# Kernel optimization log

Hardware: AMD Instinct MI355X
Metric: run time of the kernel (lower is better)

Reference implementation:

```python
import jax, jax.numpy as jnp
import numpy as np
import math

B, S, D = 4, 4096, 1024
H, DH = 16, 64          # n_heads x head_dim = d_model
INTER = 4096            # intermediate_size
CAP = int(S * 0.25)     # MoD capacity = capacity_factor * seq_len = 1024


def rmsnorm(x, w, eps=1e-6):
    return x * jax.lax.rsqrt(jnp.mean(x * x, axis=-1, keepdims=True) + eps) * w


def setup_inputs() -> dict:
    key = jax.random.key(0)
    ks = jax.random.split(key, 12)
    s = 1.0 / math.sqrt(D)
    return {
        "hidden_states": jax.random.normal(ks[0], (B, S, D), jnp.float32),
        "ssm_norm_w": jnp.ones((D,), jnp.float32),
        "ssm_a": jax.random.normal(ks[1], (D,), jnp.float32),
        "ssm_gain": jax.random.normal(ks[2], (D,), jnp.float32) * 0.1,
        "router_w": jax.random.normal(ks[3], (D,), jnp.float32) * s,
        "attn_norm_w": jnp.ones((D,), jnp.float32),
        "wq": jax.random.normal(ks[4], (D, D), jnp.float32) * s,
        "wk": jax.random.normal(ks[5], (D, D), jnp.float32) * s,
        "wv": jax.random.normal(ks[6], (D, D), jnp.float32) * s,
        "wo": jax.random.normal(ks[7], (D, D), jnp.float32) * s,
        "ffn_norm_w": jnp.ones((D,), jnp.float32),
        "w1": jax.random.normal(ks[8], (D, INTER), jnp.float32) * s,
        "w2": jax.random.normal(ks[9], (INTER, D), jnp.float32) / math.sqrt(INTER),
    }


def reference(hidden_states, ssm_norm_w, ssm_a, ssm_gain, router_w, attn_norm_w,
              wq, wk, wv, wo, ffn_norm_w, w1, w2):
    # --- SSM layer (pre-norm diagonal linear recurrence + residual) ---
    xb = rmsnorm(hidden_states, ssm_norm_w)
    decay = jax.nn.sigmoid(ssm_a)  # [D] per-channel state decay

    def step(hprev, xt):  # xt: [B, D]
        hnew = decay * hprev + (1.0 - decay) * xt
        return hnew, hnew

    _, ys = jax.lax.scan(step, jnp.zeros((B, D), jnp.float32), jnp.swapaxes(xb, 0, 1))
    h = hidden_states + jnp.swapaxes(ys, 0, 1) * ssm_gain  # [B, S, D]

    # --- MoD router: pick top-CAP tokens per sequence ---
    scores = jnp.einsum('bsd,d->bs', h, router_w)            # [B, S]
    _, idx = jax.lax.top_k(scores, CAP)                      # [B, C]
    idx = jnp.sort(idx, axis=-1)                             # keep causal order
    weights = jax.nn.sigmoid(jnp.take_along_axis(scores, idx, axis=1))  # [B, C]
    aux_loss = jnp.mean(jax.nn.sigmoid(scores))              # router load aux

    # --- gather selected tokens -> attention ---
    sel = jnp.take_along_axis(h, idx[:, :, None], axis=1)    # [B, C, D]
    xn = rmsnorm(sel, attn_norm_w)
    q = (xn @ wq).reshape(B, CAP, H, DH)
    k = (xn @ wk).reshape(B, CAP, H, DH)
    v = (xn @ wv).reshape(B, CAP, H, DH)
    att = jnp.einsum('bqhd,bkhd->bhqk', q, k) / math.sqrt(DH)
    causal = jnp.tril(jnp.ones((CAP, CAP), bool))
    att = jnp.where(causal, att, jnp.float32(-1e30))
    p = jax.nn.softmax(att, axis=-1)
    o = jnp.einsum('bhqk,bkhd->bqhd', p, v).reshape(B, CAP, D)
    attn_out = o @ wo                                        # [B, C, D]

    # --- weighted scatter_add back onto the residual stream ---
    b_idx = jnp.arange(B)[:, None]
    h = h.at[b_idx, idx].add(attn_out * weights[:, :, None])

    # --- dense FFN residual (non-MoE layer) ---
    xf = rmsnorm(h, ffn_norm_w)
    h = h + jax.nn.silu(xf @ w1) @ w2
    return h, aux_loss
```

## Files before the change

### kernel.cpp

```cpp
#include <hip/hip_runtime.h>

typedef unsigned short u16;
typedef unsigned int   u32;
typedef __attribute__((ext_vector_type(4))) float f32x4;
typedef __attribute__((ext_vector_type(8))) __bf16 bf16x8;
typedef __attribute__((ext_vector_type(8))) unsigned short u16x8;

#define DEV __device__ __forceinline__

DEV u16 f2bf(float f){
  u32 u = __builtin_bit_cast(u32, f);
  u32 r = (u + 0x7fffu + ((u >> 16) & 1u)) >> 16;
  return (u16)r;
}

DEV f32x4 mfma16(bf16x8 a, bf16x8 b, f32x4 c){
  return __builtin_amdgcn_mfma_f32_16x16x32_bf16(a, b, c, 0, 0, 0);
}

DEV void gload16(const void* g, void* l){
  __builtin_amdgcn_global_load_lds((const __attribute__((address_space(1))) u32*)g,
                                   (__attribute__((address_space(3))) u32*)l, 16, 0, 0);
}

DEV int swz16(int r, int g){ return r*64 + 8*(g ^ (r&7) ^ ((r>>3)&7)); }
DEV int swze (int r, int e){ return r*64 + (e&7) + 8*(((e>>3) ^ (r&7) ^ ((r>>3)&7))); }

__global__ __launch_bounds__(256) void transpose_cast(const float* __restrict__ src,
                                                      u16* __restrict__ dst, int R, int C){
  __shared__ float tile[32][33];
  int r  = threadIdx.x >> 3;
  int c4 = (threadIdx.x & 7) * 4;
  int r0 = blockIdx.x * 32, c0 = blockIdx.y * 32;
  float4 v = *(const float4*)&src[(size_t)(r0 + r) * C + c0 + c4];
  tile[r][c4+0] = v.x; tile[r][c4+1] = v.y; tile[r][c4+2] = v.z; tile[r][c4+3] = v.w;
  __syncthreads();
  ushort4 o;
  o.x = f2bf(tile[c4+0][r]);
  o.y = f2bf(tile[c4+1][r]);
  o.z = f2bf(tile[c4+2][r]);
  o.w = f2bf(tile[c4+3][r]);
  *(ushort4*)&dst[(size_t)(c0 + r) * R + r0 + c4] = o;
}

__global__ __launch_bounds__(256) void rms_inv_k(const float* __restrict__ x, float* __restrict__ inv){
  int row  = blockIdx.x * 4 + (threadIdx.x >> 6);
  int lane = threadIdx.x & 63;
  const float* p = x + (size_t)row * 1024;
  float ss = 0.f;
  #pragma unroll
  for (int j = 0; j < 4; ++j){
    float4 v = *(const float4*)&p[lane*4 + j*256];
    ss += v.x*v.x + v.y*v.y + v.z*v.z + v.w*v.w;
  }
  #pragma unroll
  for (int o = 1; o < 64; o <<= 1) ss += __shfl_xor(ss, o);
  if (lane == 0) inv[row] = 1.f / sqrtf(ss * (1.f/1024.f) + 1e-6f);
}

__global__ __launch_bounds__(1024) void ssm_a_k(const float* __restrict__ hid, const float* __restrict__ invr,
    const float* __restrict__ nw, const float* __restrict__ av, float* __restrict__ Fc){
  int c = blockIdx.x & 63, b = blockIdx.x >> 6;
  int d = threadIdx.x;
  float w   = nw[d];
  float dec = 1.f/(1.f + expf(-av[d]));
  float od  = 1.f - dec;
  const float* hp = hid + ((size_t)b*4096 + c*64)*1024 + d;
  const float* ip = invr + b*4096 + c*64;
  float hs = 0.f;
  for (int i = 0; i < 64; ++i)
    hs = dec*hs + od*(hp[(size_t)i*1024] * ip[i] * w);
  Fc[((size_t)b*64 + c)*1024 + d] = hs;
}
__global__ __launch_bounds__(1024) void ssm_b_k(const float* __restrict__ Fc, float* __restrict__ Init,
                                                const float* __restrict__ av){
  int b = blockIdx.x, d = threadIdx.x;
  float dec = 1.f/(1.f + expf(-av[d]));
  float dl  = powf(dec, 64.f);
  float cur = 0.f;
  for (int c = 0; c < 64; ++c){
    size_t o = ((size_t)b*64 + c)*1024 + d;
    Init[o] = cur;
    cur = dl*cur + Fc[o];
  }
}
__global__ __launch_bounds__(1024) void ssm_c_k(const float* __restrict__ hid, const float* __restrict__ invr,
    const float* __restrict__ nw, const float* __restrict__ av, const float* __restrict__ gn,
    const float* __restrict__ Init, float* __restrict__ hout){
  int c = blockIdx.x & 63, b = blockIdx.x >> 6;
  int d = threadIdx.x;
  float w   = nw[d];
  float g   = gn[d];
  float dec = 1.f/(1.f + expf(-av[d]));
  float od  = 1.f - dec;
  size_t rowoff = ((size_t)b*4096 + c*64)*1024 + d;
  const float* hp = hid + rowoff;
  float* op = hout + rowoff;
  const float* ip = invr + b*4096 + c*64;
  float hs = Init[((size_t)b*64 + c)*1024 + d];
  for (int i = 0; i < 64; ++i){
    float hv = hp[(size_t)i*1024];
    hs = dec*hs + od*(hv * ip[i] * w);
    op[(size_t)i*1024] = hv + hs*g;
  }
}

__global__ __launch_bounds__(256) void score_k(const float* __restrict__ h, const float* __restrict__ rw,
                                               float* __restrict__ sc){
  int row  = blockIdx.x * 4 + (threadIdx.x >> 6);
  int lane = threadIdx.x & 63;
  const float* p = h + (size_t)row * 1024;
  float s = 0.f;
  #pragma unroll
  for (int j = 0; j < 4; ++j){
    float4 v = *(const float4*)&p[lane*4 + j*256];
    float4 w = *(const float4*)&rw[lane*4 + j*256];
    s += v.x*w.x + v.y*w.y + v.z*w.z + v.w*w.w;
  }
  #pragma unroll
  for (int o = 1; o < 64; o <<= 1) s += __shfl_xor(s, o);
  if (lane == 0) sc[row] = s;
}

__global__ __launch_bounds__(256) void aux_k(const float* __restrict__ sc, float* __restrict__ out){
  __shared__ float red[256];
  int tid = threadIdx.x;
  float s = 0.f;
  for (int i = tid; i < 16384; i += 256) s += 1.f/(1.f + expf(-sc[i]));
  red[tid] = s; __syncthreads();
  for (int o = 128; o > 0; o >>= 1){ if (tid < o) red[tid] += red[tid+o]; __syncthreads(); }
  if (tid == 0) out[0] = red[0] * (1.f/16384.f);
}

__global__ __launch_bounds__(1024) void topk_k(const float* __restrict__ sc, int* __restrict__ idx,
                                               float* __restrict__ wsel){
  __shared__ float sv[4096];
  __shared__ int   si[4096];
  int b = blockIdx.x, tid = threadIdx.x;
  for (int i = tid; i < 4096; i += 1024){ sv[i] = sc[b*4096 + i]; si[i] = i; }
  __syncthreads();
  for (int k = 2; k <= 4096; k <<= 1)
    for (int j = k >> 1; j > 0; j >>= 1){
      for (int i = tid; i < 4096; i += 1024){
        int p = i ^ j;
        if (p > i){
          float vi = sv[i], vp = sv[p];
          int ii = si[i], ip = si[p];
          bool before = (vi > vp) || (vi == vp && ii < ip);
          bool desc = ((i & k) == 0);
          if (desc ? !before : before){ sv[i]=vp; sv[p]=vi; si[i]=ip; si[p]=ii; }
        }
      }
      __syncthreads();
    }
  for (int k = 2; k <= 1024; k <<= 1)
    for (int j = k >> 1; j > 0; j >>= 1){
      int i = tid, p = i ^ j;
      if (p > i){
        int a = si[i], c = si[p];
        bool asc = ((i & k) == 0);
        if (asc ? (a > c) : (a < c)){ si[i] = c; si[p] = a; }
      }
      __syncthreads();
    }
  int t = si[tid];
  idx[b*1024 + tid]  = t;
  wsel[b*1024 + tid] = 1.f/(1.f + expf(-sc[b*4096 + t]));
}

__global__ __launch_bounds__(256) void rownorm_bf16_k(const float* __restrict__ src, const float* __restrict__ w,
    u16* __restrict__ dst, const int* __restrict__ gidx, int base){
  int row  = blockIdx.x * 4 + (threadIdx.x >> 6);
  int lane = threadIdx.x & 63;
  size_t srow;
  if (gidx){ int b = row >> 10; srow = (size_t)b*4096 + gidx[row]; }
  else srow = (size_t)(base + row);
  const float* p = src + srow*1024;
  float4 v[4]; float ss = 0.f;
  #pragma unroll
  for (int j = 0; j < 4; ++j){
    v[j] = *(const float4*)&p[lane*4 + j*256];
    ss += v[j].x*v[j].x + v[j].y*v[j].y + v[j].z*v[j].z + v[j].w*v[j].w;
  }
  #pragma unroll
  for (int o = 1; o < 64; o <<= 1) ss += __shfl_xor(ss, o);
  float inv = 1.f / sqrtf(ss * (1.f/1024.f) + 1e-6f);
  #pragma unroll
  for (int j = 0; j < 4; ++j){
    float4 wv = *(const float4*)&w[lane*4 + j*256];
    ushort4 o4;
    o4.x = f2bf(v[j].x*inv*wv.x);
    o4.y = f2bf(v[j].y*inv*wv.y);
    o4.z = f2bf(v[j].z*inv*wv.z);
    o4.w = f2bf(v[j].w*inv*wv.w);
    *(ushort4*)&dst[(size_t)row*1024 + lane*4 + j*256] = o4;
  }
}

template<int BN, int WM, int WN, int EPI, int MINW>
__global__ __launch_bounds__(512, MINW) void gemm8(const u16* __restrict__ A, const u16* __restrict__ BT,
    u16* __restrict__ Cb, float* __restrict__ Cf, int M, int N, int K,
    const int* __restrict__ gidx, const float* __restrict__ wsel){
  constexpr int WROWS = 256 / WM;
  constexpr int WCOLS = BN / WN;
  constexpr int MI = WROWS / 16;
  constexpr int NI = WCOLS / 16;
  constexpr int BR = BN / 64;
  __shared__ u16 As[2][256*64];
  __shared__ u16 Bs[2][BN*64];

  int tid = threadIdx.x, wave = tid >> 6, lane = tid & 63;
  int lr = lane & 15, lg = lane >> 4;
  int wm = wave / WN, wn = wave % WN;

  int lin = blockIdx.x + gridDim.x * blockIdx.y;
  int nwg = gridDim.x * gridDim.y;
  int q = nwg >> 3, r = nwg & 7;
  int xc = lin & 7, of = lin >> 3;
  int s = (xc < r ? xc*(q+1) : r*(q+1) + (xc-r)*q) + of;
  int bm = s % gridDim.x, bn = s / gridDim.x;

  f32x4 zero4 = {0.f,0.f,0.f,0.f};
  f32x4 acc[MI][NI];
  #pragma unroll
  for (int mi = 0; mi < MI; ++mi)
    #pragma unroll
    for (int ni = 0; ni < NI; ++ni) acc[mi][ni] = zero4;

  int srow = (wave << 3) + (lane >> 3);
  int glog = (lane & 7) ^ (srow & 7);
  const size_t Kb = (size_t)K * 2;
  const char* aptr[4];
  const char* bptr[BR];
  #pragma unroll
  for (int rr = 0; rr < 4; ++rr)
    aptr[rr] = (const char*)A + (size_t)(bm*256 + rr*64 + srow) * Kb + glog*16;
  #pragma unroll
  for (int rr = 0; rr < BR; ++rr)
    bptr[rr] = (const char*)BT + (size_t)(bn*BN + rr*64 + srow) * Kb + glog*16;

  int nkt = K >> 6;
  #pragma unroll
  for (int rr = 0; rr < 4; ++rr) gload16(aptr[rr], &As[0][(rr*64 + (wave<<3))*64]);
  #pragma unroll
  for (int rr = 0; rr < BR; ++rr) gload16(bptr[rr], &Bs[0][(rr*64 + (wave<<3))*64]);
  __syncthreads();

  for (int kt = 0; kt < nkt; ++kt){
    int bi = kt & 1;
    if (kt + 1 < nkt){
      size_t koff = (size_t)(kt + 1) << 7;
      #pragma unroll
      for (int rr = 0; rr < 4; ++rr) gload16(aptr[rr] + koff, &As[bi^1][(rr*64 + (wave<<3))*64]);
      #pragma unroll
      for (int rr = 0; rr < BR; ++rr) gload16(bptr[rr] + koff, &Bs[bi^1][(rr*64 + (wave<<3))*64]);
    }
    __builtin_amdgcn_sched_barrier(0);

    bf16x8 bfrag[NI][2];
    #pragma unroll
    for (int ni = 0; ni < NI; ++ni)
      #pragma unroll
      for (int ks = 0; ks < 2; ++ks){
        int row = wn*WCOLS + ni*16 + lr;
        int gl = (ks*4 + lg) ^ (row & 7);
        bfrag[ni][ks] = *(const bf16x8*)&Bs[bi][row*64 + gl*8];
      }
    #pragma unroll
    for (int mh = 0; mh < 2; ++mh){
      bf16x8 afrag[MI/2][2];
      #pragma unroll
      for (int i = 0; i < MI/2; ++i)
        #pragma unroll
        for (int ks = 0; ks < 2; ++ks){
          int row = wm*WROWS + (mh*(MI/2) + i)*16 + lr;
          int gl = (ks*4 + lg) ^ (row & 7);
          afrag[i][ks] = *(const bf16x8*)&As[bi][row*64 + gl*8];
        }
      #pragma unroll
      for (int i = 0; i < MI/2; ++i)
        #pragma unroll
        for (int ni = 0; ni < NI; ++ni){
          f32x4 a = acc[mh*(MI/2)+i][ni];
          a = mfma16(afrag[i][0], bfrag[ni][0], a);
          a = mfma16(afrag[i][1], bfrag[ni][1], a);
          acc[mh*(MI/2)+i][ni] = a;
        }
    }
    __syncthreads();
  }

  #pragma unroll
  for (int mi = 0; mi < MI; ++mi){
    int rb = bm*256 + wm*WROWS + mi*16 + lg*4;
    #pragma unroll
    for (int ni = 0; ni < NI; ++ni){
      int col = bn*BN + wn*WCOLS + ni*16 + lr;
      f32x4 v = acc[mi][ni];
      if constexpr (EPI == 0){
        #pragma unroll
        for (int t = 0; t < 4; ++t) Cb[(size_t)(rb+t)*N + col] = f2bf(v[t]);
      } else if constexpr (EPI == 1){
        #pragma unroll
        for (int t = 0; t < 4; ++t){ float x = v[t]; Cb[(size_t)(rb+t)*N + col] = f2bf(x / (1.f + expf(-x))); }
      } else if constexpr (EPI == 2){
        #pragma unroll
        for (int t = 0; t < 4; ++t) Cf[(size_t)(rb+t)*N + col] += v[t];
      } else {
        #pragma unroll
        for (int t = 0; t < 4; ++t){
          int rr = rb + t;
          int bb = rr >> 10;
          float* hr = Cf + ((size_t)bb*4096 + gidx[rr])*1024;
          hr[col] += v[t] * wsel[rr];
        }
      }
    }
  }
}

DEV void attn_body(const u16* __restrict__ qkv, u16* __restrict__ obuf,
                   u16* Ks, u16* Vt, u16* Pl, int b, int hh, int qt){
  int tid = threadIdx.x;
  int wave = tid >> 6, lane = tid & 63;
  int lr = lane & 15, lg = lane >> 4;

  const u16* qrow = qkv + (size_t)(b*1024 + qt*64 + wave*16 + lr)*3072 + hh*64;
  bf16x8 qf0 = *(const bf16x8*)(qrow + lg*8);
  bf16x8 qf1 = *(const bf16x8*)(qrow + 32 + lg*8);

  f32x4 zero4 = {0.f,0.f,0.f,0.f};
  f32x4 oacc[4];
  #pragma unroll
  for (int d = 0; d < 4; ++d) oacc[d] = zero4;
  float m[4], s[4];
  #pragma unroll
  for (int t = 0; t < 4; ++t){ m[t] = -INFINITY; s[t] = 0.f; }

  int key0 = tid >> 3,         ce0 = (tid & 7) * 8;
  int key1 = (tid + 256) >> 3, ce1 = ((tid + 256) & 7) * 8;
  u16x8 kreg0, kreg1, vreg0, vreg1;

  const u16* kvbase = qkv + (size_t)(b*1024)*3072 + 1024 + hh*64;
  {
    const u16* g0 = kvbase + (size_t)key0*3072 + ce0;
    const u16* g1 = kvbase + (size_t)key1*3072 + ce1;
    kreg0 = *(const u16x8*)g0;  vreg0 = *(const u16x8*)(g0 + 1024);
    kreg1 = *(const u16x8*)g1;  vreg1 = *(const u16x8*)(g1 + 1024);
  }

  for (int kt = 0; kt <= qt; ++kt){
    __syncthreads();
    *(u16x8*)&Ks[swz16(key0, ce0 >> 3)] = kreg0;
    *(u16x8*)&Ks[swz16(key1, ce1 >> 3)] = kreg1;
    #pragma unroll
    for (int j = 0; j < 8; ++j) Vt[swze(ce0 + j, key0)] = vreg0[j];
    #pragma unroll
    for (int j = 0; j < 8; ++j) Vt[swze(ce1 + j, key1)] = vreg1[j];
    __syncthreads();
    if (kt < qt){
      const u16* g0 = kvbase + (size_t)((kt+1)*64 + key0)*3072 + ce0;
      const u16* g1 = kvbase + (size_t)((kt+1)*64 + key1)*3072 + ce1;
      kreg0 = *(const u16x8*)g0;  vreg0 = *(const u16x8*)(g0 + 1024);
      kreg1 = *(const u16x8*)g1;  vreg1 = *(const u16x8*)(g1 + 1024);
    }

    float sv[4][4];
    #pragma unroll
    for (int kb = 0; kb < 4; ++kb){
      f32x4 sa = zero4;
      bf16x8 k0f = *(const bf16x8*)&Ks[swz16(kb*16 + lr, lg)];
      bf16x8 k1f = *(const bf16x8*)&Ks[swz16(kb*16 + lr, 4 + lg)];
      sa = mfma16(qf0, k0f, sa);
      sa = mfma16(qf1, k1f, sa);
      #pragma unroll
      for (int t = 0; t < 4; ++t) sv[kb][t] = sa[t]*0.125f;
    }
    if (kt == qt){
      #pragma unroll
      for (int kb = 0; kb < 4; ++kb){
        int keyg = kb*16 + lr;
        #pragma unroll
        for (int t = 0; t < 4; ++t){
          int qg = wave*16 + lg*4 + t;
          if (keyg > qg) sv[kb][t] = -1e30f;
        }
      }
    }
    float mn[4], scale[4];
    #pragma unroll
    for (int t = 0; t < 4; ++t){
      float tm = fmaxf(fmaxf(sv[0][t], sv[1][t]), fmaxf(sv[2][t], sv[3][t]));
      #pragma unroll
      for (int o = 1; o < 16; o <<= 1) tm = fmaxf(tm, __shfl_xor(tm, o));
      mn[t] = fmaxf(m[t], tm);
      scale[t] = expf(m[t] - mn[t]);
      m[t] = mn[t];
    }
    float ps[4] = {0.f,0.f,0.f,0.f};
    #pragma unroll
    for (int kb = 0; kb < 4; ++kb)
      #pragma unroll
      for (int t = 0; t < 4; ++t){
        float p = expf(sv[kb][t] - mn[t]);
        ps[t] += p;
        Pl[wave*1024 + swze(lg*4 + t, kb*16 + lr)] = f2bf(p);
      }
    #pragma unroll
    for (int t = 0; t < 4; ++t){
      #pragma unroll
      for (int o = 1; o < 16; o <<= 1) ps[t] += __shfl_xor(ps[t], o);
      s[t] = s[t]*scale[t] + ps[t];
    }
    #pragma unroll
    for (int d = 0; d < 4; ++d){
      f32x4 v = oacc[d];
      #pragma unroll
      for (int t = 0; t < 4; ++t) v[t] *= scale[t];
      oacc[d] = v;
    }
    bf16x8 pa0 = *(const bf16x8*)&Pl[wave*1024 + swz16(lr, lg)];
    bf16x8 pa1 = *(const bf16x8*)&Pl[wave*1024 + swz16(lr, 4 + lg)];
    #pragma unroll
    for (int d = 0; d < 4; ++d){
      bf16x8 v0 = *(const bf16x8*)&Vt[swz16(d*16 + lr, lg)];
      bf16x8 v1 = *(const bf16x8*)&Vt[swz16(d*16 + lr, 4 + lg)];
      oacc[d] = mfma16(pa0, v0, oacc[d]);
      oacc[d] = mfma16(pa1, v1, oacc[d]);
    }
  }
  #pragma unroll
  for (int d = 0; d < 4; ++d)
    #pragma unroll
    for (int t = 0; t < 4; ++t){
      int qrel = qt*64 + wave*16 + lg*4 + t;
      float val = oacc[d][t] / s[t];
      obuf[(size_t)(b*1024 + qrel)*1024 + hh*64 + d*16 + lr] = f2bf(val);
    }
}

__global__ __launch_bounds__(256) void attn_k(const u16* __restrict__ qkv, u16* __restrict__ obuf){
  __shared__ u16 Ks[64*64];
  __shared__ u16 Vt[64*64];
  __shared__ u16 Pl[4*16*64];
  int blk = blockIdx.x;
  int qp = blk & 7;
  int hh = (blk >> 3) & 15;
  int b  = blk >> 7;
  attn_body(qkv, obuf, Ks, Vt, Pl, b, hh, qp);
  attn_body(qkv, obuf, Ks, Vt, Pl, b, hh, 15 - qp);
}

extern "C" void kernel_launch(void* const* d_in, const int* in_sizes, int n_in,
                              void* d_out, int out_size, void* d_ws, size_t ws_size,
                              hipStream_t stream) {
  const float* hid    = (const float*)d_in[0];
  const float* nssm   = (const float*)d_in[1];
  const float* ssma   = (const float*)d_in[2];
  const float* ssmg   = (const float*)d_in[3];
  const float* routw  = (const float*)d_in[4];
  const float* nattn  = (const float*)d_in[5];
  const float* wq     = (const float*)d_in[6];
  const float* wk     = (const float*)d_in[7];
  const float* wv     = (const float*)d_in[8];
  const float* wo     = (const float*)d_in[9];
  const float* nffn   = (const float*)d_in[10];
  const float* w1     = (const float*)d_in[11];
  const float* w2     = (const float*)d_in[12];

  float* hbuf = (float*)d_out;
  char* wsb = (char*)d_ws;
  u16*   wqkvT  = (u16*)(wsb + 0);
  u16*   woT    = (u16*)(wsb + 6291456);
  u16*   w1T    = (u16*)(wsb + 8388608);
  u16*   w2T    = (u16*)(wsb + 16777216);
  float* invr   = (float*)(wsb + 25165824);
  float* scores = (float*)(wsb + 25231360);
  float* Fc     = (float*)(wsb + 25296896);
  float* Init   = (float*)(wsb + 26345472);
  int*   idxb   = (int*)(wsb + 27394048);
  float* wselb  = (float*)(wsb + 27410432);
  u16*   xn     = (u16*)(wsb + 27426816);
  u16*   qkv    = (u16*)(wsb + 35815424);
  u16*   obuf   = (u16*)(wsb + 60981248);
  u16*   xf     = (u16*)(wsb + 27394048);
  u16*   act    = (u16*)(wsb + 35782656);

  transpose_cast<<<dim3(32,32),  256, 0, stream>>>(wq, wqkvT,              1024, 1024);
  transpose_cast<<<dim3(32,32),  256, 0, stream>>>(wk, wqkvT + 1048576,    1024, 1024);
  transpose_cast<<<dim3(32,32),  256, 0, stream>>>(wv, wqkvT + 2097152,    1024, 1024);
  transpose_cast<<<dim3(32,32),  256, 0, stream>>>(wo, woT,                1024, 1024);
  transpose_cast<<<dim3(32,128), 256, 0, stream>>>(w1, w1T,                1024, 4096);
  transpose_cast<<<dim3(128,32), 256, 0, stream>>>(w2, w2T,                4096, 1024);

  rms_inv_k<<<4096, 256, 0, stream>>>(hid, invr);
  ssm_a_k<<<256, 1024, 0, stream>>>(hid, invr, nssm, ssma, Fc);
  ssm_b_k<<<4,   1024, 0, stream>>>(Fc, Init, ssma);
  ssm_c_k<<<256, 1024, 0, stream>>>(hid, invr, nssm, ssma, ssmg, Init, hbuf);

  score_k<<<4096, 256, 0, stream>>>(hbuf, routw, scores);
  aux_k<<<1, 256, 0, stream>>>(scores, hbuf + 16777216);
  topk_k<<<4, 1024, 0, stream>>>(scores, idxb, wselb);

  rownorm_bf16_k<<<1024, 256, 0, stream>>>(hbuf, nattn, xn, idxb, 0);
  gemm8<256,2,4,0,2><<<dim3(16,12), 512, 0, stream>>>(xn, wqkvT, qkv, nullptr, 4096, 3072, 1024, nullptr, nullptr);
  attn_k<<<512, 256, 0, stream>>>(qkv, obuf);
  gemm8<64,4,2,3,4><<<dim3(16,16), 512, 0, stream>>>(obuf, woT, nullptr, hbuf, 4096, 1024, 1024, idxb, wselb);

  for (int ch = 0; ch < 4; ++ch){
    int m0 = ch * 4096;
    rownorm_bf16_k<<<1024, 256, 0, stream>>>(hbuf, nffn, xf, nullptr, m0);
    gemm8<256,2,4,1,2><<<dim3(16,16), 512, 0, stream>>>(xf, w1T, act, nullptr, 4096, 4096, 1024, nullptr, nullptr);
    gemm8<64,4,2,2,4><<<dim3(16,16), 512, 0, stream>>>(act, w2T, nullptr, hbuf + (size_t)m0*1024, 4096, 1024, 4096, nullptr, nullptr);
  }
  (void)in_sizes; (void)n_in; (void)out_size; (void)ws_size;
}
```

Measured before the change: 829.8 us.

## Triple-buffer GEMM pipeline, retile GEMMs, and parallel-scan SSM chunk carry

The GEMM kernel moves from double- to triple-buffered LDS staging. Explicit vmcnt waits and raw s_barrier keep two k-tiles in flight, and s_setprio raises priority around the MFMA block. Each GEMM launch gets new tile shapes (BM/BN templated, 128x128 or 256x128), and all A fragments are loaded at once. The SSM chunk-carry kernel becomes a wave-level Hillis-Steele scan over the 64 chunks across 256 blocks instead of a serial loop in 4 blocks. The costs are higher LDS and register use, which can lower occupancy, and a slightly different floating-point rounding order in the scan.

```diff
diff --git a/kernel.cpp b/kernel.cpp
--- a/kernel.cpp
+++ b/kernel.cpp
@@ -22,6 +22,8 @@
   __builtin_amdgcn_global_load_lds((const __attribute__((address_space(1))) u32*)g,
                                    (__attribute__((address_space(3))) u32*)l, 16, 0, 0);
 }
+
+template<int N> DEV void waitvm(){ asm volatile("s_waitcnt vmcnt(%0)" :: "n"(N) : "memory"); }
 
 DEV int swz16(int r, int g){ return r*64 + 8*(g ^ (r&7) ^ ((r>>3)&7)); }
 DEV int swze (int r, int e){ return r*64 + (e&7) + 8*(((e>>3) ^ (r&7) ^ ((r>>3)&7))); }
@@ -74,15 +76,23 @@
 }
 __global__ __launch_bounds__(1024) void ssm_b_k(const float* __restrict__ Fc, float* __restrict__ Init,
                                                 const float* __restrict__ av){
-  int b = blockIdx.x, d = threadIdx.x;
+  int b  = blockIdx.x >> 6;
+  int dg = blockIdx.x & 63;
+  int dl = threadIdx.x >> 6;
+  int c  = threadIdx.x & 63;
+  int d  = dg*16 + dl;
   float dec = 1.f/(1.f + expf(-av[d]));
-  float dl  = powf(dec, 64.f);
-  float cur = 0.f;
-  for (int c = 0; c < 64; ++c){
-    size_t o = ((size_t)b*64 + c)*1024 + d;
-    Init[o] = cur;
-    cur = dl*cur + Fc[o];
-  }
+  float a = powf(dec, 64.f);
+  float x = Fc[((size_t)(b*64 + c))*1024 + d];
+  float coef = a;
+  #pragma unroll
+  for (int s = 1; s < 64; s <<= 1){
+    float prev = __shfl_up(x, s, 64);
+    if (c >= s) x += coef * prev;
+    coef *= coef;
+  }
+  float ex = __shfl_up(x, 1, 64);
+  Init[((size_t)(b*64 + c))*1024 + d] = (c > 0) ? ex : 0.f;
 }
 __global__ __launch_bounds__(1024) void ssm_c_k(const float* __restrict__ hid, const float* __restrict__ invr,
     const float* __restrict__ nw, const float* __restrict__ av, const float* __restrict__ gn,
@@ -197,17 +207,19 @@
   }
 }
 
-template<int BN, int WM, int WN, int EPI, int MINW>
-__global__ __launch_bounds__(512, MINW) void gemm8(const u16* __restrict__ A, const u16* __restrict__ BT,
+template<int BM, int BN, int WM, int WN, int EPI>
+__global__ __launch_bounds__(512, 1) void gemmp(const u16* __restrict__ A, const u16* __restrict__ BT,
     u16* __restrict__ Cb, float* __restrict__ Cf, int M, int N, int K,
     const int* __restrict__ gidx, const float* __restrict__ wsel){
-  constexpr int WROWS = 256 / WM;
+  constexpr int WROWS = BM / WM;
   constexpr int WCOLS = BN / WN;
   constexpr int MI = WROWS / 16;
   constexpr int NI = WCOLS / 16;
+  constexpr int AR = BM / 64;
   constexpr int BR = BN / 64;
-  __shared__ u16 As[2][256*64];
-  __shared__ u16 Bs[2][BN*64];
+  constexpr int LPS = AR + BR;
+  __shared__ u16 As[3][BM*64];
+  __shared__ u16 Bs[3][BN*64];
 
   int tid = threadIdx.x, wave = tid >> 6, lane = tid & 63;
   int lr = lane & 15, lg = lane >> 4;
@@ -215,10 +227,10 @@
 
   int lin = blockIdx.x + gridDim.x * blockIdx.y;
   int nwg = gridDim.x * gridDim.y;
-  int q = nwg >> 3, r = nwg & 7;
+  int q8 = nwg >> 3, r8 = nwg & 7;
   int xc = lin & 7, of = lin >> 3;
-  int s = (xc < r ? xc*(q+1) : r*(q+1) + (xc-r)*q) + of;
-  int bm = s % gridDim.x, bn = s / gridDim.x;
+  int sw = (xc < r8 ? xc*(q8+1) : r8*(q8+1) + (xc-r8)*q8) + of;
+  int bm = sw % gridDim.x, bn = sw / gridDim.x;
 
   f32x4 zero4 = {0.f,0.f,0.f,0.f};
   f32x4 acc[MI][NI];
@@ -230,32 +242,34 @@
   int srow = (wave << 3) + (lane >> 3);
   int glog = (lane & 7) ^ (srow & 7);
   const size_t Kb = (size_t)K * 2;
-  const char* aptr[4];
+  const char* aptr[AR];
   const char* bptr[BR];
   #pragma unroll
-  for (int rr = 0; rr < 4; ++rr)
-    aptr[rr] = (const char*)A + (size_t)(bm*256 + rr*64 + srow) * Kb + glog*16;
+  for (int rr = 0; rr < AR; ++rr)
+    aptr[rr] = (const char*)A + (size_t)(bm*BM + rr*64 + srow) * Kb + glog*16;
   #pragma unroll
   for (int rr = 0; rr < BR; ++rr)
     bptr[rr] = (const char*)BT + (size_t)(bn*BN + rr*64 + srow) * Kb + glog*16;
 
   int nkt = K >> 6;
-  #pragma unroll
-  for (int rr = 0; rr < 4; ++rr) gload16(aptr[rr], &As[0][(rr*64 + (wave<<3))*64]);
-  #pragma unroll
-  for (int rr = 0; rr < BR; ++rr) gload16(bptr[rr], &Bs[0][(rr*64 + (wave<<3))*64]);
-  __syncthreads();
-
-  for (int kt = 0; kt < nkt; ++kt){
-    int bi = kt & 1;
-    if (kt + 1 < nkt){
-      size_t koff = (size_t)(kt + 1) << 7;
-      #pragma unroll
-      for (int rr = 0; rr < 4; ++rr) gload16(aptr[rr] + koff, &As[bi^1][(rr*64 + (wave<<3))*64]);
-      #pragma unroll
-      for (int rr = 0; rr < BR; ++rr) gload16(bptr[rr] + koff, &Bs[bi^1][(rr*64 + (wave<<3))*64]);
-    }
-    __builtin_amdgcn_sched_barrier(0);
+
+#define STAGE(T, BUF) do { \
+    size_t koff = (size_t)(T) << 7; \
+    _Pragma("unroll") \
+    for (int rr = 0; rr < AR; ++rr) gload16(aptr[rr] + koff, &As[BUF][(rr*64 + (wave<<3))*64]); \
+    _Pragma("unroll") \
+    for (int rr = 0; rr < BR; ++rr) gload16(bptr[rr] + koff, &Bs[BUF][(rr*64 + (wave<<3))*64]); \
+  } while(0)
+
+  STAGE(0, 0);
+  STAGE(1, 1);
+
+  for (int t = 0; t < nkt; ++t){
+    int q = t % 3;
+    if (t + 2 < nkt){ STAGE(t+2, (t+2)%3); waitvm<2*LPS>(); }
+    else if (t + 1 < nkt){ waitvm<LPS>(); }
+    else { waitvm<0>(); }
+    __builtin_amdgcn_s_barrier();
 
     bf16x8 bfrag[NI][2];
     #pragma unroll
@@ -264,35 +278,35 @@
       for (int ks = 0; ks < 2; ++ks){
         int row = wn*WCOLS + ni*16 + lr;
         int gl = (ks*4 + lg) ^ (row & 7);
-        bfrag[ni][ks] = *(const bf16x8*)&Bs[bi][row*64 + gl*8];
-      }
-    #pragma unroll
-    for (int mh = 0; mh < 2; ++mh){
-      bf16x8 afrag[MI/2][2];
-      #pragma unroll
-      for (int i = 0; i < MI/2; ++i)
-        #pragma unroll
-        for (int ks = 0; ks < 2; ++ks){
-          int row = wm*WROWS + (mh*(MI/2) + i)*16 + lr;
-          int gl = (ks*4 + lg) ^ (row & 7);
-          afrag[i][ks] = *(const bf16x8*)&As[bi][row*64 + gl*8];
-        }
-      #pragma unroll
-      for (int i = 0; i < MI/2; ++i)
-        #pragma unroll
-        for (int ni = 0; ni < NI; ++ni){
-          f32x4 a = acc[mh*(MI/2)+i][ni];
-          a = mfma16(afrag[i][0], bfrag[ni][0], a);
-          a = mfma16(afrag[i][1], bfrag[ni][1], a);
-          acc[mh*(MI/2)+i][ni] = a;
-        }
-    }
-    __syncthreads();
-  }
+        bfrag[ni][ks] = *(const bf16x8*)&Bs[q][row*64 + gl*8];
+      }
+    bf16x8 afrag[MI][2];
+    #pragma unroll
+    for (int mi = 0; mi < MI; ++mi)
+      #pragma unroll
+      for (int ks = 0; ks < 2; ++ks){
+        int row = wm*WROWS + mi*16 + lr;
+        int gl = (ks*4 + lg) ^ (row & 7);
+        afrag[mi][ks] = *(const bf16x8*)&As[q][row*64 + gl*8];
+      }
+    __builtin_amdgcn_s_setprio(1);
+    #pragma unroll
+    for (int mi = 0; mi < MI; ++mi)
+      #pragma unroll
+      for (int ni = 0; ni < NI; ++ni){
+        f32x4 a = acc[mi][ni];
+        a = mfma16(afrag[mi][0], bfrag[ni][0], a);
+        a = mfma16(afrag[mi][1], bfrag[ni][1], a);
+        acc[mi][ni] = a;
+      }
+    __builtin_amdgcn_s_setprio(0);
+    __builtin_amdgcn_s_barrier();
+  }
+#undef STAGE
 
   #pragma unroll
   for (int mi = 0; mi < MI; ++mi){
-    int rb = bm*256 + wm*WROWS + mi*16 + lg*4;
+    int rb = bm*BM + wm*WROWS + mi*16 + lg*4;
     #pragma unroll
     for (int ni = 0; ni < NI; ++ni){
       int col = bn*BN + wn*WCOLS + ni*16 + lr;
@@ -495,7 +509,7 @@
 
   rms_inv_k<<<4096, 256, 0, stream>>>(hid, invr);
   ssm_a_k<<<256, 1024, 0, stream>>>(hid, invr, nssm, ssma, Fc);
-  ssm_b_k<<<4,   1024, 0, stream>>>(Fc, Init, ssma);
+  ssm_b_k<<<256, 1024, 0, stream>>>(Fc, Init, ssma);
   ssm_c_k<<<256, 1024, 0, stream>>>(hid, invr, nssm, ssma, ssmg, Init, hbuf);
 
   score_k<<<4096, 256, 0, stream>>>(hbuf, routw, scores);
@@ -503,15 +517,15 @@
   topk_k<<<4, 1024, 0, stream>>>(scores, idxb, wselb);
 
   rownorm_bf16_k<<<1024, 256, 0, stream>>>(hbuf, nattn, xn, idxb, 0);
-  gemm8<256,2,4,0,2><<<dim3(16,12), 512, 0, stream>>>(xn, wqkvT, qkv, nullptr, 4096, 3072, 1024, nullptr, nullptr);
+  gemmp<128,128,2,4,0><<<dim3(32,24), 512, 0, stream>>>(xn, wqkvT, qkv, nullptr, 4096, 3072, 1024, nullptr, nullptr);
   attn_k<<<512, 256, 0, stream>>>(qkv, obuf);
-  gemm8<64,4,2,3,4><<<dim3(16,16), 512, 0, stream>>>(obuf, woT, nullptr, hbuf, 4096, 1024, 1024, idxb, wselb);
+  gemmp<128,128,2,4,3><<<dim3(32,8), 512, 0, stream>>>(obuf, woT, nullptr, hbuf, 4096, 1024, 1024, idxb, wselb);
 
   for (int ch = 0; ch < 4; ++ch){
     int m0 = ch * 4096;
     rownorm_bf16_k<<<1024, 256, 0, stream>>>(hbuf, nffn, xf, nullptr, m0);
-    gemm8<256,2,4,1,2><<<dim3(16,16), 512, 0, stream>>>(xf, w1T, act, nullptr, 4096, 4096, 1024, nullptr, nullptr);
-    gemm8<64,4,2,2,4><<<dim3(16,16), 512, 0, stream>>>(act, w2T, nullptr, hbuf + (size_t)m0*1024, 4096, 1024, 4096, nullptr, nullptr);
+    gemmp<256,128,4,2,1><<<dim3(16,32), 512, 0, stream>>>(xf, w1T, act, nullptr, 4096, 4096, 1024, nullptr, nullptr);
+    gemmp<128,128,2,4,2><<<dim3(32,8), 512, 0, stream>>>(act, w2T, nullptr, hbuf + (size_t)m0*1024, 4096, 1024, 4096, nullptr, nullptr);
   }
   (void)in_sizes; (void)n_in; (void)out_size; (void)ws_size;
 }
```

After: 874.9 us. 1.05x slower.

## Add deep-pipelined FFN up GEMM, parallel SSM chunk scan, and K-from-global attention

Applied to the files above, without the earlier changes.

Adds a new GEMM kernel for the W1 projection. It uses four K-slice LDS stages with counted vmcnt waits and raised MFMA priority, so loads stay in flight while compute runs. The SSM carry pass changes from a 4-block serial loop into a 256-block wave-shuffle parallel scan over chunks. Attention now reads K fragments directly from global memory instead of staging them in LDS, and triple-buffers V in LDS to drop one barrier per tile. The risks are more global traffic for K in attention and higher register pressure in the new GEMM.

```diff
diff --git a/kernel.cpp b/kernel.cpp
--- a/kernel.cpp
+++ b/kernel.cpp
@@ -22,6 +22,8 @@
   __builtin_amdgcn_global_load_lds((const __attribute__((address_space(1))) u32*)g,
                                    (__attribute__((address_space(3))) u32*)l, 16, 0, 0);
 }
+
+template<int N> DEV void waitvm(){ asm volatile("s_waitcnt vmcnt(%0)" :: "n"(N) : "memory"); }
 
 DEV int swz16(int r, int g){ return r*64 + 8*(g ^ (r&7) ^ ((r>>3)&7)); }
 DEV int swze (int r, int e){ return r*64 + (e&7) + 8*(((e>>3) ^ (r&7) ^ ((r>>3)&7))); }
@@ -74,15 +76,23 @@
 }
 __global__ __launch_bounds__(1024) void ssm_b_k(const float* __restrict__ Fc, float* __restrict__ Init,
                                                 const float* __restrict__ av){
-  int b = blockIdx.x, d = threadIdx.x;
+  int b  = blockIdx.x >> 6;
+  int dg = blockIdx.x & 63;
+  int dl = threadIdx.x >> 6;
+  int c  = threadIdx.x & 63;
+  int d  = dg*16 + dl;
   float dec = 1.f/(1.f + expf(-av[d]));
-  float dl  = powf(dec, 64.f);
-  float cur = 0.f;
-  for (int c = 0; c < 64; ++c){
-    size_t o = ((size_t)b*64 + c)*1024 + d;
-    Init[o] = cur;
-    cur = dl*cur + Fc[o];
-  }
+  float a = powf(dec, 64.f);
+  float x = Fc[((size_t)(b*64 + c))*1024 + d];
+  float coef = a;
+  #pragma unroll
+  for (int s = 1; s < 64; s <<= 1){
+    float prev = __shfl_up(x, s, 64);
+    if (c >= s) x += coef * prev;
+    coef *= coef;
+  }
+  float ex = __shfl_up(x, 1, 64);
+  Init[((size_t)(b*64 + c))*1024 + d] = (c > 0) ? ex : 0.f;
 }
 __global__ __launch_bounds__(1024) void ssm_c_k(const float* __restrict__ hid, const float* __restrict__ invr,
     const float* __restrict__ nw, const float* __restrict__ av, const float* __restrict__ gn,
@@ -215,10 +225,10 @@
 
   int lin = blockIdx.x + gridDim.x * blockIdx.y;
   int nwg = gridDim.x * gridDim.y;
-  int q = nwg >> 3, r = nwg & 7;
+  int q8 = nwg >> 3, r8 = nwg & 7;
   int xc = lin & 7, of = lin >> 3;
-  int s = (xc < r ? xc*(q+1) : r*(q+1) + (xc-r)*q) + of;
-  int bm = s % gridDim.x, bn = s / gridDim.x;
+  int sw = (xc < r8 ? xc*(q8+1) : r8*(q8+1) + (xc-r8)*q8) + of;
+  int bm = sw % gridDim.x, bn = sw / gridDim.x;
 
   f32x4 zero4 = {0.f,0.f,0.f,0.f};
   f32x4 acc[MI][NI];
@@ -319,8 +329,113 @@
   }
 }
 
+template<int EPI>
+__global__ __launch_bounds__(512, 2) void gemmdp(const u16* __restrict__ A, const u16* __restrict__ BT,
+    u16* __restrict__ Cb, float* __restrict__ Cf, int M, int N, int K,
+    const int* __restrict__ gidx, const float* __restrict__ wsel){
+  __shared__ u16 As[2][2][256*32];
+  __shared__ u16 Bs[2][2][256*32];
+  int tid = threadIdx.x, wave = tid >> 6, lane = tid & 63;
+  int lr = lane & 15, lg = lane >> 4;
+  int wm = wave >> 2, wn = wave & 3;
+
+  int lin = blockIdx.x + gridDim.x * blockIdx.y;
+  int nwg = gridDim.x * gridDim.y;
+  int q8 = nwg >> 3, r8 = nwg & 7;
+  int xc = lin & 7, of = lin >> 3;
+  int sw = (xc < r8 ? xc*(q8+1) : r8*(q8+1) + (xc-r8)*q8) + of;
+  int bm = sw % gridDim.x, bn = sw / gridDim.x;
+
+  f32x4 zero4 = {0.f,0.f,0.f,0.f};
+  f32x4 acc[8][4];
+  #pragma unroll
+  for (int mi = 0; mi < 8; ++mi)
+    #pragma unroll
+    for (int ni = 0; ni < 4; ++ni) acc[mi][ni] = zero4;
+
+  int sr = lane >> 2;
+  int sg = lane & 3;
+  const size_t Kb = (size_t)K * 2;
+  const char* abase[2]; const char* bbase[2];
+  #pragma unroll
+  for (int rr = 0; rr < 2; ++rr){
+    int ga = bm*256 + rr*128 + wave*16 + sr;
+    int gb = bn*256 + rr*128 + wave*16 + sr;
+    abase[rr] = (const char*)A  + (size_t)ga * Kb + (sg ^ (ga & 3))*16;
+    bbase[rr] = (const char*)BT + (size_t)gb * Kb + (sg ^ (gb & 3))*16;
+  }
+  int NP = K >> 5;
+
+#define STG(Q) do { \
+    int _b = ((Q)>>1)&1, _s = (Q)&1; \
+    size_t _ko = (size_t)(Q) << 6; \
+    gload16(abase[0] + _ko, &As[_b][_s][(wave*16)*32]); \
+    gload16(abase[1] + _ko, &As[_b][_s][(128 + wave*16)*32]); \
+    gload16(bbase[0] + _ko, &Bs[_b][_s][(wave*16)*32]); \
+    gload16(bbase[1] + _ko, &Bs[_b][_s][(128 + wave*16)*32]); \
+  } while(0)
+
+#define PHASE(P, NW) do { \
+    waitvm<NW>(); \
+    __builtin_amdgcn_s_barrier(); \
+    __builtin_amdgcn_sched_barrier(0); \
+    const u16* _Asl = &As[((P)>>1)&1][(P)&1][0]; \
+    const u16* _Bsl = &Bs[((P)>>1)&1][(P)&1][0]; \
+    bf16x8 bfrag[4]; \
+    _Pragma("unroll") \
+    for (int ni = 0; ni < 4; ++ni){ \
+      int row = wn*64 + ni*16 + lr; \
+      bfrag[ni] = *(const bf16x8*)&_Bsl[row*32 + ((lg ^ (row & 3))*8)]; \
+    } \
+    bf16x8 afrag[8]; \
+    _Pragma("unroll") \
+    for (int mi = 0; mi < 8; ++mi){ \
+      int row = wm*128 + mi*16 + lr; \
+      afrag[mi] = *(const bf16x8*)&_Asl[row*32 + ((lg ^ (row & 3))*8)]; \
+    } \
+    __builtin_amdgcn_s_setprio(1); \
+    _Pragma("unroll") \
+    for (int mi = 0; mi < 8; ++mi) \
+      _Pragma("unroll") \
+      for (int ni = 0; ni < 4; ++ni) \
+        acc[mi][ni] = mfma16(afrag[mi], bfrag[ni], acc[mi][ni]); \
+    __builtin_amdgcn_s_setprio(0); \
+    __builtin_amdgcn_sched_barrier(0); \
+    __builtin_amdgcn_s_barrier(); \
+  } while(0)
+
+  STG(0); STG(1); STG(2);
+  int P = 0;
+  for (; P < NP - 3; ++P){ STG(P+3); PHASE(P, 12); }
+  PHASE(P, 8);  ++P;
+  PHASE(P, 4);  ++P;
+  PHASE(P, 0);
+#undef STG
+#undef PHASE
+
+  #pragma unroll
+  for (int mi = 0; mi < 8; ++mi){
+    int rb = bm*256 + wm*128 + mi*16 + lg*4;
+    #pragma unroll
+    for (int ni = 0; ni < 4; ++ni){
+      int col = bn*256 + wn*64 + ni*16 + lr;
+      f32x4 v = acc[mi][ni];
+      if constexpr (EPI == 0){
+        #pragma unroll
+        for (int t = 0; t < 4; ++t) Cb[(size_t)(rb+t)*N + col] = f2bf(v[t]);
+      } else if constexpr (EPI == 1){
+        #pragma unroll
+        for (int t = 0; t < 4; ++t){ float x = v[t]; Cb[(size_t)(rb+t)*N + col] = f2bf(x / (1.f + expf(-x))); }
+      } else {
+        #pragma unroll
+        for (int t = 0; t < 4; ++t) Cf[(size_t)(rb+t)*N + col] += v[t];
+      }
+    }
+  }
+}
+
 DEV void attn_body(const u16* __restrict__ qkv, u16* __restrict__ obuf,
-                   u16* Ks, u16* Vt, u16* Pl, int b, int hh, int qt){
+                   u16 (*Vt)[4096], u16* Pl, int b, int hh, int qt){
   int tid = threadIdx.x;
   int wave = tid >> 6, lane = tid & 63;
   int lr = lane & 15, lg = lane >> 4;
@@ -339,38 +454,32 @@
 
   int key0 = tid >> 3,         ce0 = (tid & 7) * 8;
   int key1 = (tid + 256) >> 3, ce1 = ((tid + 256) & 7) * 8;
-  u16x8 kreg0, kreg1, vreg0, vreg1;
-
-  const u16* kvbase = qkv + (size_t)(b*1024)*3072 + 1024 + hh*64;
-  {
-    const u16* g0 = kvbase + (size_t)key0*3072 + ce0;
-    const u16* g1 = kvbase + (size_t)key1*3072 + ce1;
-    kreg0 = *(const u16x8*)g0;  vreg0 = *(const u16x8*)(g0 + 1024);
-    kreg1 = *(const u16x8*)g1;  vreg1 = *(const u16x8*)(g1 + 1024);
-  }
+  u16x8 vreg0, vreg1;
+
+  const u16* kbase = qkv + (size_t)(b*1024)*3072 + 1024 + hh*64;
+  const u16* vbase = kbase + 1024;
+  vreg0 = *(const u16x8*)(vbase + (size_t)key0*3072 + ce0);
+  vreg1 = *(const u16x8*)(vbase + (size_t)key1*3072 + ce1);
 
   for (int kt = 0; kt <= qt; ++kt){
-    __syncthreads();
-    *(u16x8*)&Ks[swz16(key0, ce0 >> 3)] = kreg0;
-    *(u16x8*)&Ks[swz16(key1, ce1 >> 3)] = kreg1;
-    #pragma unroll
-    for (int j = 0; j < 8; ++j) Vt[swze(ce0 + j, key0)] = vreg0[j];
-    #pragma unroll
-    for (int j = 0; j < 8; ++j) Vt[swze(ce1 + j, key1)] = vreg1[j];
+    u16* Vb = Vt[kt % 3];
+    #pragma unroll
+    for (int j = 0; j < 8; ++j) Vb[swze(ce0 + j, key0)] = vreg0[j];
+    #pragma unroll
+    for (int j = 0; j < 8; ++j) Vb[swze(ce1 + j, key1)] = vreg1[j];
     __syncthreads();
     if (kt < qt){
-      const u16* g0 = kvbase + (size_t)((kt+1)*64 + key0)*3072 + ce0;
-      const u16* g1 = kvbase + (size_t)((kt+1)*64 + key1)*3072 + ce1;
-      kreg0 = *(const u16x8*)g0;  vreg0 = *(const u16x8*)(g0 + 1024);
-      kreg1 = *(const u16x8*)g1;  vreg1 = *(const u16x8*)(g1 + 1024);
+      vreg0 = *(const u16x8*)(vbase + (size_t)((kt+1)*64 + key0)*3072 + ce0);
+      vreg1 = *(const u16x8*)(vbase + (size_t)((kt+1)*64 + key1)*3072 + ce1);
     }
 
     float sv[4][4];
     #pragma unroll
     for (int kb = 0; kb < 4; ++kb){
+      const u16* krow = kbase + (size_t)(kt*64 + kb*16 + lr)*3072;
+      bf16x8 k0f = *(const bf16x8*)(krow + lg*8);
+      bf16x8 k1f = *(const bf16x8*)(krow + 32 + lg*8);
       f32x4 sa = zero4;
-      bf16x8 k0f = *(const bf16x8*)&Ks[swz16(kb*16 + lr, lg)];
-      bf16x8 k1f = *(const bf16x8*)&Ks[swz16(kb*16 + lr, 4 + lg)];
       sa = mfma16(qf0, k0f, sa);
       sa = mfma16(qf1, k1f, sa);
       #pragma unroll
@@ -423,8 +532,8 @@
     bf16x8 pa1 = *(const bf16x8*)&Pl[wave*1024 + swz16(lr, 4 + lg)];
     #pragma unroll
     for (int d = 0; d < 4; ++d){
-      bf16x8 v0 = *(const bf16x8*)&Vt[swz16(d*16 + lr, lg)];
-      bf16x8 v1 = *(const bf16x8*)&Vt[swz16(d*16 + lr, 4 + lg)];
+      bf16x8 v0 = *(const bf16x8*)&Vb[swz16(d*16 + lr, lg)];
+      bf16x8 v1 = *(const bf16x8*)&Vb[swz16(d*16 + lr, 4 + lg)];
       oacc[d] = mfma16(pa0, v0, oacc[d]);
       oacc[d] = mfma16(pa1, v1, oacc[d]);
     }
@@ -439,16 +548,16 @@
     }
 }
 
-__global__ __launch_bounds__(256) void attn_k(const u16* __restrict__ qkv, u16* __restrict__ obuf){
-  __shared__ u16 Ks[64*64];
-  __shared__ u16 Vt[64*64];
+__global__ __launch_bounds__(256, 4) void attn_k(const u16* __restrict__ qkv, u16* __restrict__ obuf){
+  __shared__ u16 Vt[3][4096];
   __shared__ u16 Pl[4*16*64];
   int blk = blockIdx.x;
   int qp = blk & 7;
   int hh = (blk >> 3) & 15;
   int b  = blk >> 7;
-  attn_body(qkv, obuf, Ks, Vt, Pl, b, hh, qp);
-  attn_body(qkv, obuf, Ks, Vt, Pl, b, hh, 15 - qp);
+  attn_body(qkv, obuf, Vt, Pl, b, hh, qp);
+  __syncthreads();
+  attn_body(qkv, obuf, Vt, Pl, b, hh, 15 - qp);
 }
 
 extern "C" void kernel_launch(void* const* d_in, const int* in_sizes, int n_in,
@@ -495,7 +604,7 @@
 
   rms_inv_k<<<4096, 256, 0, stream>>>(hid, invr);
   ssm_a_k<<<256, 1024, 0, stream>>>(hid, invr, nssm, ssma, Fc);
-  ssm_b_k<<<4,   1024, 0, stream>>>(Fc, Init, ssma);
+  ssm_b_k<<<256, 1024, 0, stream>>>(Fc, Init, ssma);
   ssm_c_k<<<256, 1024, 0, stream>>>(hid, invr, nssm, ssma, ssmg, Init, hbuf);
 
   score_k<<<4096, 256, 0, stream>>>(hbuf, routw, scores);
@@ -510,7 +619,7 @@
   for (int ch = 0; ch < 4; ++ch){
     int m0 = ch * 4096;
     rownorm_bf16_k<<<1024, 256, 0, stream>>>(hbuf, nffn, xf, nullptr, m0);
-    gemm8<256,2,4,1,2><<<dim3(16,16), 512, 0, stream>>>(xf, w1T, act, nullptr, 4096, 4096, 1024, nullptr, nullptr);
+    gemmdp<1><<<dim3(16,16), 512, 0, stream>>>(xf, w1T, act, nullptr, 4096, 4096, 1024, nullptr, nullptr);
     gemm8<64,4,2,2,4><<<dim3(16,16), 512, 0, stream>>>(act, w2T, nullptr, hbuf + (size_t)m0*1024, 4096, 1024, 4096, nullptr, nullptr);
   }
   (void)in_sizes; (void)n_in; (void)out_size; (void)ws_size;
```

After: 953.6 us. 1.15x slower.
